# Optimization experiments

Hardware: AMD Instinct MI355X
Metric: run time of the kernel (lower is better)

## Reference

```python
import jax, jax.numpy as jnp
import numpy as np


def setup_inputs() -> dict:
    key = jax.random.key(0)
    ks = jax.random.split(key, 8)
    N, E, D, R = 50000, 1000000, 64, 64
    H = 2 * D  # hidden = 128
    return {
        "node_feats": jax.random.normal(ks[0], (N, D), dtype=jnp.float32),
        "edge_feats": jax.random.normal(ks[1], (E, R), dtype=jnp.float32),
        "src_idx": jax.random.randint(ks[2], (E,), 0, N, dtype=jnp.int32),
        "dst_idx": jax.random.randint(ks[3], (E,), 0, N, dtype=jnp.int32),
        "W1": jax.random.normal(ks[4], (2 * D + R, H), dtype=jnp.float32) * (1.0 / np.sqrt(2 * D + R)),
        "b1": jnp.zeros((H,), dtype=jnp.float32),
        "W2": jax.random.normal(ks[5], (H, R), dtype=jnp.float32) * (1.0 / np.sqrt(H)),
        "b2": jnp.zeros((R,), dtype=jnp.float32),
    }


def reference(node_feats, edge_feats, src_idx, dst_idx, W1, b1, W2, b2):
    # Per-edge gather of src/dst node features, concat with edge rbf: [E, 2D+R]
    h_src = node_feats[src_idx]                 # [E, D]
    h_dst = node_feats[dst_idx]                 # [E, D]
    edge_h = jnp.concatenate([h_src, h_dst, edge_feats], axis=-1)  # [E, 2D+R]
    # 2-layer MLP with Softplus activation
    hidden = jax.nn.softplus(edge_h @ W1 + b1)  # [E, 2D]
    out = hidden @ W2 + b2                      # [E, R]
    return out
```

## Files before the change

### kernel.cpp

```cpp
#include <hip/hip_runtime.h>
#include <hip/hip_bf16.h>

typedef __bf16 bf16x8 __attribute__((ext_vector_type(8)));
typedef __bf16 bf16x4_t __attribute__((ext_vector_type(4)));
typedef short s16x4 __attribute__((ext_vector_type(4)));
typedef float f32x4 __attribute__((ext_vector_type(4)));
typedef unsigned int u32;

static __device__ __forceinline__ f32x4 mfma32(bf16x8 a, bf16x8 b, f32x4 c) {
    return __builtin_amdgcn_mfma_f32_16x16x32_bf16(a, b, c, 0, 0, 0);
}

static __device__ __forceinline__ f32x4 mfma16(s16x4 a, s16x4 b, f32x4 c) {
#if __has_builtin(__builtin_amdgcn_mfma_f32_16x16x16bf16_1k)
    return __builtin_amdgcn_mfma_f32_16x16x16bf16_1k(a, b, c, 0, 0, 0);
#elif __has_builtin(__builtin_amdgcn_mfma_f32_16x16x16_bf16)
    return __builtin_amdgcn_mfma_f32_16x16x16_bf16(
        __builtin_bit_cast(bf16x4_t, a), __builtin_bit_cast(bf16x4_t, b), c, 0, 0, 0);
#else
    asm volatile("s_nop 1\n\tv_mfma_f32_16x16x16_bf16 %0, %1, %2, %0\n\ts_nop 7\n\ts_nop 7"
                 : "+v"(c) : "v"(a), "v"(b));
    return c;
#endif
}

static __device__ __forceinline__ u32 packsp(float x0, float x1) {
    float s0 = fmaxf(x0, 0.f) + __logf(1.f + __expf(-fabsf(x0)));
    float s1 = fmaxf(x1, 0.f) + __logf(1.f + __expf(-fabsf(x1)));
    union { __bf16 b[2]; u32 w; } u;
    u.b[0] = (__bf16)s0; u.b[1] = (__bf16)s1;
    return u.w;
}

static __device__ __forceinline__ s16x4 mk4(u32 lo, u32 hi) {
    union { u32 w[2]; s16x4 v; } u;
    u.w[0] = lo; u.w[1] = hi;
    return u.v;
}

__global__ __launch_bounds__(512, 4) void edge_mlp_kernel(
    const float* __restrict__ node_feats,
    const float* __restrict__ edge_feats,
    const int* __restrict__ src_idx,
    const int* __restrict__ dst_idx,
    const float* __restrict__ W1,
    const float* __restrict__ b1,
    const float* __restrict__ W2,
    const float* __restrict__ b2,
    float* __restrict__ out,
    int E, int nchunks)
{
    __shared__ alignas(16) __bf16 sW1f[8 * 6 * 64 * 8];
    __shared__ alignas(16) __bf16 sW2f[4 * 4 * 64 * 8];
    __shared__ alignas(16) __bf16 sB1f[8 * 64 * 4];
    __shared__ alignas(16) __bf16 sB2f[4 * 64 * 4];

    const int tid  = threadIdx.x;
    const int lane = tid & 63;
    const int wid  = tid >> 6;

    for (int i = tid; i < 192 * 128; i += 512) {
        int k = i >> 7, h = i & 127;
        int n = h >> 4, r = h & 15, t = k >> 5, kq = (k >> 3) & 3, j = k & 7;
        sW1f[((n * 6 + t) * 64 + kq * 16 + r) * 8 + j] = (__bf16)W1[i];
    }
    for (int i = tid; i < 128 * 64; i += 512) {
        int h = i >> 6, r = i & 63;
        int rt = r >> 4, r16 = r & 15, n = h >> 4, hq = (h >> 2) & 3, j = h & 3;
        sW2f[((rt * 4 + (n >> 1)) * 64 + hq * 16 + r16) * 8 + (n & 1) * 4 + j] = (__bf16)W2[i];
    }
    for (int s = tid; s < 8 * 64 * 4; s += 512) {
        int j = s & 3, ln = (s >> 2) & 63, n = s >> 8;
        sB1f[s] = (j == 0 && ln < 16) ? (__bf16)b1[n * 16 + ln] : (__bf16)0.f;
    }
    for (int s = tid; s < 4 * 64 * 4; s += 512) {
        int j = s & 3, ln = (s >> 2) & 63, rt = s >> 8;
        sB2f[s] = (j == 0 && ln < 16) ? (__bf16)b2[rt * 16 + ln] : (__bf16)0.f;
    }
    __syncthreads();

    const int q   = lane >> 4;
    const int r16 = lane & 15;
    const int ko  = q * 8;

    const __bf16* w1p = &sW1f[lane * 8];
    const __bf16* w2p = &sW2f[lane * 8];
    const __bf16* b1p = &sB1f[lane * 4];
    const __bf16* b2p = &sB2f[lane * 4];

    const s16x4 one = {(short)(q == 0 ? 0x3F80 : 0), 0, 0, 0};

    int c = blockIdx.x;
    u32 os0, od0, oe0, os1, od1, oe1;
    {
        int b = c * 256 + wid * 32;
        int e0 = b + r16, e1 = b + 16 + r16;
        int ie0 = e0 < E ? e0 : E - 1;
        int ie1 = e1 < E ? e1 : E - 1;
        os0 = (u32)src_idx[ie0] * 64 + ko; od0 = (u32)dst_idx[ie0] * 64 + ko;
        os1 = (u32)src_idx[ie1] * 64 + ko; od1 = (u32)dst_idx[ie1] * 64 + ko;
        oe0 = (u32)ie0 * 64 + ko;          oe1 = (u32)ie1 * 64 + ko;
    }

#define LOAD_T(T, B) {                                                          \
        u32 oo0 = (T < 2) ? os0 + T * 32 : (T < 4) ? od0 + (T - 2) * 32 : oe0 + (T - 4) * 32; \
        u32 oo1 = (T < 2) ? os1 + T * 32 : (T < 4) ? od1 + (T - 2) * 32 : oe1 + (T - 4) * 32; \
        const float* bp = (T < 4) ? node_feats : edge_feats;                    \
        B[0] = *(const f32x4*)(bp + oo0); B[1] = *(const f32x4*)(bp + oo0 + 4); \
        B[2] = *(const f32x4*)(bp + oo1); B[3] = *(const f32x4*)(bp + oo1 + 4); }

#define STEP_T(T, CUR, NXT) {                                                   \
        if (T < 5) LOAD_T(T + 1, NXT);                                          \
        bf16x8 ef0, ef1;                                                        \
        _Pragma("unroll")                                                       \
        for (int j = 0; j < 4; ++j) {                                           \
            ef0[j] = (__bf16)CUR[0][j]; ef0[j + 4] = (__bf16)CUR[1][j];         \
            ef1[j] = (__bf16)CUR[2][j]; ef1[j + 4] = (__bf16)CUR[3][j];         \
        }                                                                       \
        _Pragma("unroll")                                                       \
        for (int n = 0; n < 8; ++n) {                                           \
            bf16x8 w = *(const bf16x8*)(w1p + (n * 6 + T) * 512);               \
            acc1[0][n] = mfma32(w, ef0, acc1[0][n]);                            \
            acc1[1][n] = mfma32(w, ef1, acc1[1][n]);                            \
        }                                                                       \
        __builtin_amdgcn_sched_barrier(0); }

    while (c < nchunks) {
        const int base = c * 256 + wid * 32;

        const int cn = c + gridDim.x;
        int nis0 = 0, nid0 = 0, nis1 = 0, nid1 = 0, nie0 = 0, nie1 = 0;
        if (cn < nchunks) {
            int bb = cn * 256 + wid * 32;
            int e0 = bb + r16, e1 = bb + 16 + r16;
            nie0 = e0 < E ? e0 : E - 1;
            nie1 = e1 < E ? e1 : E - 1;
            nis0 = src_idx[nie0]; nid0 = dst_idx[nie0];
            nis1 = src_idx[nie1]; nid1 = dst_idx[nie1];
        }

        f32x4 acc1[2][8];
#pragma unroll
        for (int m = 0; m < 2; ++m)
#pragma unroll
            for (int n = 0; n < 8; ++n) acc1[m][n] = (f32x4){0.f, 0.f, 0.f, 0.f};

        f32x4 bufA[4], bufB[4];
        LOAD_T(0, bufA);
        STEP_T(0, bufA, bufB);
        STEP_T(1, bufB, bufA);
        STEP_T(2, bufA, bufB);
        STEP_T(3, bufB, bufA);
        STEP_T(4, bufA, bufB);
        STEP_T(5, bufB, bufA);

#pragma unroll
        for (int n = 0; n < 8; ++n) {
            s16x4 wb = *(const s16x4*)(b1p + n * 256);
            acc1[0][n] = mfma16(wb, one, acc1[0][n]);
            acc1[1][n] = mfma16(wb, one, acc1[1][n]);
        }

        u32 P[2][8][2];
#pragma unroll
        for (int m = 0; m < 2; ++m)
#pragma unroll
            for (int n = 0; n < 8; ++n) {
                P[m][n][0] = packsp(acc1[m][n][0], acc1[m][n][1]);
                P[m][n][1] = packsp(acc1[m][n][2], acc1[m][n][3]);
            }

        const int e0 = base + r16, e1 = base + 16 + r16;
        float* op0 = out + (size_t)e0 * 64 + q * 4;
        float* op1 = out + (size_t)e1 * 64 + q * 4;
#pragma unroll
        for (int rt = 0; rt < 4; ++rt) {
            f32x4 a20 = {0.f, 0.f, 0.f, 0.f};
            f32x4 a21 = {0.f, 0.f, 0.f, 0.f};
#pragma unroll
            for (int np = 0; np < 4; ++np) {
                union { bf16x8 v8; s16x4 h[2]; } uw;
                uw.v8 = *(const bf16x8*)(w2p + (rt * 4 + np) * 512);
                a20 = mfma16(uw.h[0], mk4(P[0][2 * np][0],     P[0][2 * np][1]),     a20);
                a20 = mfma16(uw.h[1], mk4(P[0][2 * np + 1][0], P[0][2 * np + 1][1]), a20);
                a21 = mfma16(uw.h[0], mk4(P[1][2 * np][0],     P[1][2 * np][1]),     a21);
                a21 = mfma16(uw.h[1], mk4(P[1][2 * np + 1][0], P[1][2 * np + 1][1]), a21);
            }
            s16x4 wb2 = *(const s16x4*)(b2p + rt * 256);
            a20 = mfma16(wb2, one, a20);
            a21 = mfma16(wb2, one, a21);
            if (e0 < E) *(f32x4*)(op0 + rt * 16) = a20;
            if (e1 < E) *(f32x4*)(op1 + rt * 16) = a21;
        }

        if (cn < nchunks) {
            os0 = (u32)nis0 * 64 + ko; od0 = (u32)nid0 * 64 + ko;
            os1 = (u32)nis1 * 64 + ko; od1 = (u32)nid1 * 64 + ko;
            oe0 = (u32)nie0 * 64 + ko; oe1 = (u32)nie1 * 64 + ko;
        }
        c = cn;
    }
#undef LOAD_T
#undef STEP_T
}

extern "C" void kernel_launch(void* const* d_in, const int* in_sizes, int n_in,
                              void* d_out, int out_size, void* d_ws, size_t ws_size,
                              hipStream_t stream) {
    const float* node_feats = (const float*)d_in[0];
    const float* edge_feats = (const float*)d_in[1];
    const int*   src_idx    = (const int*)d_in[2];
    const int*   dst_idx    = (const int*)d_in[3];
    const float* W1         = (const float*)d_in[4];
    const float* b1         = (const float*)d_in[5];
    const float* W2         = (const float*)d_in[6];
    const float* b2         = (const float*)d_in[7];
    float* out = (float*)d_out;

    const int E = in_sizes[2];
    const int nchunks = (E + 255) / 256;
    int grid = nchunks < 512 ? nchunks : 512;

    edge_mlp_kernel<<<grid, 512, 0, stream>>>(node_feats, edge_feats, src_idx, dst_idx,
                                              W1, b1, W2, b2, out, E, nchunks);
}
```

Baseline: 180.5 us.

## Triple-buffer gather loads and prefetch next chunk's first tiles across layer-2

Replaces the double-buffered per-tile gather with a three-buffer rotation that issues loads two K-steps ahead. The first two tiles of the next chunk are loaded during the second MLP layer and the output stores, hiding gather latency across iterations. Softplus is also simplified to log(1+exp(x)), which saves a few ALU ops. That form can overflow to inf for large inputs. The extra buffers raise register pressure, which may affect occupancy at 512 threads and 4 blocks.

```diff
diff --git a/kernel.cpp b/kernel.cpp
--- a/kernel.cpp
+++ b/kernel.cpp
@@ -25,8 +25,8 @@
 }
 
 static __device__ __forceinline__ u32 packsp(float x0, float x1) {
-    float s0 = fmaxf(x0, 0.f) + __logf(1.f + __expf(-fabsf(x0)));
-    float s1 = fmaxf(x1, 0.f) + __logf(1.f + __expf(-fabsf(x1)));
+    float s0 = __logf(1.f + __expf(x0));
+    float s1 = __logf(1.f + __expf(x1));
     union { __bf16 b[2]; u32 w; } u;
     u.b[0] = (__bf16)s0; u.b[1] = (__bf16)s1;
     return u.w;
@@ -90,8 +90,33 @@
 
     const s16x4 one = {(short)(q == 0 ? 0x3F80 : 0), 0, 0, 0};
 
+#define TOFF(T, S, Dd, Ee) ((T) < 2 ? (S) + (T) * 32 : (T) < 4 ? (Dd) + ((T) - 2) * 32 : (Ee) + ((T) - 4) * 32)
+
+#define GL(T, B, S0, D0, E0o, S1, D1, E1o) {                                    \
+        u32 a0 = TOFF(T, S0, D0, E0o), a1 = TOFF(T, S1, D1, E1o);               \
+        const float* bp = ((T) < 4) ? node_feats : edge_feats;                  \
+        B[0] = *(const f32x4*)(bp + a0); B[1] = *(const f32x4*)(bp + a0 + 4);   \
+        B[2] = *(const f32x4*)(bp + a1); B[3] = *(const f32x4*)(bp + a1 + 4); }
+
+#define STEP(T, CUR, LD) {                                                      \
+        if ((T) < 4) GL((T) + 2, LD, os0, od0, oe0, os1, od1, oe1);             \
+        bf16x8 ef0, ef1;                                                        \
+        _Pragma("unroll")                                                       \
+        for (int j = 0; j < 4; ++j) {                                           \
+            ef0[j] = (__bf16)CUR[0][j]; ef0[j + 4] = (__bf16)CUR[1][j];         \
+            ef1[j] = (__bf16)CUR[2][j]; ef1[j + 4] = (__bf16)CUR[3][j];         \
+        }                                                                       \
+        _Pragma("unroll")                                                       \
+        for (int n = 0; n < 8; ++n) {                                           \
+            bf16x8 w = *(const bf16x8*)(w1p + (n * 6 + (T)) * 512);             \
+            acc1[0][n] = mfma32(w, ef0, acc1[0][n]);                            \
+            acc1[1][n] = mfma32(w, ef1, acc1[1][n]);                            \
+        }                                                                       \
+        __builtin_amdgcn_sched_barrier(0); }
+
     int c = blockIdx.x;
     u32 os0, od0, oe0, os1, od1, oe1;
+    f32x4 G0[4], G1[4], G2[4];
     {
         int b = c * 256 + wid * 32;
         int e0 = b + r16, e1 = b + 16 + r16;
@@ -100,43 +125,23 @@
         os0 = (u32)src_idx[ie0] * 64 + ko; od0 = (u32)dst_idx[ie0] * 64 + ko;
         os1 = (u32)src_idx[ie1] * 64 + ko; od1 = (u32)dst_idx[ie1] * 64 + ko;
         oe0 = (u32)ie0 * 64 + ko;          oe1 = (u32)ie1 * 64 + ko;
-    }
-
-#define LOAD_T(T, B) {                                                          \
-        u32 oo0 = (T < 2) ? os0 + T * 32 : (T < 4) ? od0 + (T - 2) * 32 : oe0 + (T - 4) * 32; \
-        u32 oo1 = (T < 2) ? os1 + T * 32 : (T < 4) ? od1 + (T - 2) * 32 : oe1 + (T - 4) * 32; \
-        const float* bp = (T < 4) ? node_feats : edge_feats;                    \
-        B[0] = *(const f32x4*)(bp + oo0); B[1] = *(const f32x4*)(bp + oo0 + 4); \
-        B[2] = *(const f32x4*)(bp + oo1); B[3] = *(const f32x4*)(bp + oo1 + 4); }
-
-#define STEP_T(T, CUR, NXT) {                                                   \
-        if (T < 5) LOAD_T(T + 1, NXT);                                          \
-        bf16x8 ef0, ef1;                                                        \
-        _Pragma("unroll")                                                       \
-        for (int j = 0; j < 4; ++j) {                                           \
-            ef0[j] = (__bf16)CUR[0][j]; ef0[j + 4] = (__bf16)CUR[1][j];         \
-            ef1[j] = (__bf16)CUR[2][j]; ef1[j + 4] = (__bf16)CUR[3][j];         \
-        }                                                                       \
-        _Pragma("unroll")                                                       \
-        for (int n = 0; n < 8; ++n) {                                           \
-            bf16x8 w = *(const bf16x8*)(w1p + (n * 6 + T) * 512);               \
-            acc1[0][n] = mfma32(w, ef0, acc1[0][n]);                            \
-            acc1[1][n] = mfma32(w, ef1, acc1[1][n]);                            \
-        }                                                                       \
-        __builtin_amdgcn_sched_barrier(0); }
+        GL(0, G0, os0, od0, oe0, os1, od1, oe1);
+        GL(1, G1, os0, od0, oe0, os1, od1, oe1);
+    }
 
     while (c < nchunks) {
         const int base = c * 256 + wid * 32;
 
         const int cn = c + gridDim.x;
-        int nis0 = 0, nid0 = 0, nis1 = 0, nid1 = 0, nie0 = 0, nie1 = 0;
+        u32 nos0 = os0, nod0 = od0, noe0 = oe0, nos1 = os1, nod1 = od1, noe1 = oe1;
         if (cn < nchunks) {
             int bb = cn * 256 + wid * 32;
             int e0 = bb + r16, e1 = bb + 16 + r16;
-            nie0 = e0 < E ? e0 : E - 1;
-            nie1 = e1 < E ? e1 : E - 1;
-            nis0 = src_idx[nie0]; nid0 = dst_idx[nie0];
-            nis1 = src_idx[nie1]; nid1 = dst_idx[nie1];
+            int nie0 = e0 < E ? e0 : E - 1;
+            int nie1 = e1 < E ? e1 : E - 1;
+            nos0 = (u32)src_idx[nie0] * 64 + ko; nod0 = (u32)dst_idx[nie0] * 64 + ko;
+            nos1 = (u32)src_idx[nie1] * 64 + ko; nod1 = (u32)dst_idx[nie1] * 64 + ko;
+            noe0 = (u32)nie0 * 64 + ko;          noe1 = (u32)nie1 * 64 + ko;
         }
 
         f32x4 acc1[2][8];
@@ -145,14 +150,12 @@
 #pragma unroll
             for (int n = 0; n < 8; ++n) acc1[m][n] = (f32x4){0.f, 0.f, 0.f, 0.f};
 
-        f32x4 bufA[4], bufB[4];
-        LOAD_T(0, bufA);
-        STEP_T(0, bufA, bufB);
-        STEP_T(1, bufB, bufA);
-        STEP_T(2, bufA, bufB);
-        STEP_T(3, bufB, bufA);
-        STEP_T(4, bufA, bufB);
-        STEP_T(5, bufB, bufA);
+        STEP(0, G0, G2);
+        STEP(1, G1, G0);
+        STEP(2, G2, G1);
+        STEP(3, G0, G2);
+        STEP(4, G1, G1);
+        STEP(5, G2, G2);
 
 #pragma unroll
         for (int n = 0; n < 8; ++n) {
@@ -169,6 +172,12 @@
                 P[m][n][0] = packsp(acc1[m][n][0], acc1[m][n][1]);
                 P[m][n][1] = packsp(acc1[m][n][2], acc1[m][n][3]);
             }
+        __builtin_amdgcn_sched_barrier(0);
+
+        if (cn < nchunks) {
+            GL(0, G0, nos0, nod0, noe0, nos1, nod1, noe1);
+            GL(1, G1, nos0, nod0, noe0, nos1, nod1, noe1);
+        }
 
         const int e0 = base + r16, e1 = base + 16 + r16;
         float* op0 = out + (size_t)e0 * 64 + q * 4;
@@ -193,15 +202,13 @@
             if (e1 < E) *(f32x4*)(op1 + rt * 16) = a21;
         }
 
-        if (cn < nchunks) {
-            os0 = (u32)nis0 * 64 + ko; od0 = (u32)nid0 * 64 + ko;
-            os1 = (u32)nis1 * 64 + ko; od1 = (u32)nid1 * 64 + ko;
-            oe0 = (u32)nie0 * 64 + ko; oe1 = (u32)nie1 * 64 + ko;
-        }
+        os0 = nos0; od0 = nod0; oe0 = noe0;
+        os1 = nos1; od1 = nod1; oe1 = noe1;
         c = cn;
     }
-#undef LOAD_T
-#undef STEP_T
+#undef STEP
+#undef GL
+#undef TOFF
 }
 
 extern "C" void kernel_launch(void* const* d_in, const int* in_sizes, int n_in,
```

New measurement: 293.7 us. 62.8% more time.
